# Kernel tuning notes

Measured on AMD Instinct MI355X. Metric: run time of the kernel, lower is better.

Reference implementation:

```python
import jax, jax.numpy as jnp
import numpy as np

IN_FEATURES = 4096
OUT_FEATURES = 11008
B, S = 4, 2048


def setup_inputs() -> dict:
    key = jax.random.key(0)
    k1, k2, k3, k4 = jax.random.split(key, 4)
    x = jax.random.normal(k1, (B, S, IN_FEATURES), dtype=jnp.float32)
    # int8 quantized weights in [-127, 127]
    weight_quantized = jax.random.randint(k2, (OUT_FEATURES, IN_FEATURES), -127, 128, dtype=jnp.int8)
    # realistic per-channel scales (positive, small)
    weight_scale = jax.random.uniform(k3, (OUT_FEATURES,), dtype=jnp.float32, minval=1e-4, maxval=2e-2)
    bias = jax.random.normal(k4, (OUT_FEATURES,), dtype=jnp.float32) * 0.01
    return {"x": x, "weight_quantized": weight_quantized, "weight_scale": weight_scale, "bias": bias}


def reference(x, weight_quantized, weight_scale, bias):
    # Dequantize: W = int8.float() * scale[:, None]  (symmetric, per-channel)
    w = weight_quantized.astype(jnp.float32) * weight_scale[:, None]  # [out, in]
    # F.linear: y = x @ W^T + b
    return jnp.einsum('bsi,oi->bso', x, w) + bias
```

## Files before the change

### kernel.cpp

```cpp
#include <hip/hip_runtime.h>
#include <hip/hip_bf16.h>
#include <stdint.h>


#define M_TOTAL 8192
#define K_TOTAL 4096
#define N_TOTAL 11008
#define NT 32
#define NBM 64
#define NBN 86

typedef __attribute__((ext_vector_type(4))) int int4v;

__device__ inline ushort f2bf(float f) {
    union { __hip_bfloat16 h; ushort u; } cv;
    cv.h = __float2bfloat16(f);
    return cv.u;
}


__global__ __launch_bounds__(256) void quant_x_kernel(const float* __restrict__ x,
                                                      signed char* __restrict__ xq,
                                                      float* __restrict__ sx) {
    const int row = blockIdx.x;
    const int tid = threadIdx.x;
    const float* xr = x + (size_t)row * K_TOTAL + tid * 16;

    float4 v0 = reinterpret_cast<const float4*>(xr)[0];
    float4 v1 = reinterpret_cast<const float4*>(xr)[1];
    float4 v2 = reinterpret_cast<const float4*>(xr)[2];
    float4 v3 = reinterpret_cast<const float4*>(xr)[3];

    float m = 0.f;
    m = fmaxf(m, fmaxf(fmaxf(fabsf(v0.x), fabsf(v0.y)), fmaxf(fabsf(v0.z), fabsf(v0.w))));
    m = fmaxf(m, fmaxf(fmaxf(fabsf(v1.x), fabsf(v1.y)), fmaxf(fabsf(v1.z), fabsf(v1.w))));
    m = fmaxf(m, fmaxf(fmaxf(fabsf(v2.x), fabsf(v2.y)), fmaxf(fabsf(v2.z), fabsf(v2.w))));
    m = fmaxf(m, fmaxf(fmaxf(fabsf(v3.x), fabsf(v3.y)), fmaxf(fabsf(v3.z), fabsf(v3.w))));

    for (int d = 1; d < 64; d <<= 1) m = fmaxf(m, __shfl_xor(m, d));
    __shared__ float wm_[4];
    if ((tid & 63) == 0) wm_[tid >> 6] = m;
    __syncthreads();
    m = fmaxf(fmaxf(wm_[0], wm_[1]), fmaxf(wm_[2], wm_[3]));

    const float inv = (m > 0.f) ? (127.f / m) : 0.f;
    if (tid == 0) sx[row] = (m > 0.f) ? (m / 127.f) : 0.f;

    float tmp[16] = {v0.x,v0.y,v0.z,v0.w, v1.x,v1.y,v1.z,v1.w,
                     v2.x,v2.y,v2.z,v2.w, v3.x,v3.y,v3.z,v3.w};
    int q[16];
#pragma unroll
    for (int i = 0; i < 16; ++i) {
        int t = __float2int_rn(tmp[i] * inv);
        q[i] = t > 127 ? 127 : (t < -127 ? -127 : t);
    }
    int4v o;
#pragma unroll
    for (int w = 0; w < 4; ++w)
        o[w] = (q[w*4] & 255) | ((q[w*4+1] & 255) << 8) |
               ((q[w*4+2] & 255) << 16) | ((q[w*4+3] & 255) << 24);
    *reinterpret_cast<int4v*>(xq + (size_t)row * K_TOTAL + tid * 16) = o;
}


__global__ __launch_bounds__(256) void cvt_w_kernel(const int* __restrict__ in,
                                                    signed char* __restrict__ out, int nitems) {
    bool is8 = false;
    for (int i = 0; i < 256; ++i) {
        int v = in[i];
        if (v < -127 || v > 127) { is8 = true; break; }
    }
    int stride = gridDim.x * blockDim.x;
    if (!is8) {
        for (int i = blockIdx.x * blockDim.x + threadIdx.x; i < nitems; i += stride) {
            const int* p = in + (size_t)i * 16;
            int4v o;
#pragma unroll
            for (int w = 0; w < 4; ++w)
                o[w] = (p[w*4] & 255) | ((p[w*4+1] & 255) << 8) |
                       ((p[w*4+2] & 255) << 16) | ((p[w*4+3] & 255) << 24);
            *reinterpret_cast<int4v*>(out + (size_t)i * 16) = o;
        }
    } else {
        const int4v* in16 = reinterpret_cast<const int4v*>(in);
        for (int i = blockIdx.x * blockDim.x + threadIdx.x; i < nitems; i += stride)
            *reinterpret_cast<int4v*>(out + (size_t)i * 16) = in16[i];
    }
}


#define GLOAD16(g, l) __builtin_amdgcn_global_load_lds( \
    (const __attribute__((address_space(1))) void*)(g), \
    (__attribute__((address_space(3))) void*)(l), 16, 0, 0)


__global__ __launch_bounds__(256, 2) void gemm_kernel(const unsigned char* __restrict__ A,
                                                      const unsigned char* __restrict__ B,
                                                      const float* __restrict__ sx,
                                                      const float* __restrict__ scale,
                                                      const float* __restrict__ bias,
                                                      float* __restrict__ C) {
    __shared__ unsigned char sh[65536];

    const int tid  = threadIdx.x;
    const int wv   = tid >> 6;
    const int lane = tid & 63;
    const int wm   = wv >> 1;
    const int wn   = wv & 1;

    const int xcd = blockIdx.x & 7;
    const int l   = blockIdx.x >> 3;
    const int band = l / 344;
    const int lb   = l - band * 344;
    const int st   = lb >> 4;
    const int r    = lb & 15;
    int bm_l, bn;
    if (st < 21) { bm_l = band * 4 + (r >> 2); bn = st * 4 + (r & 3); }
    else         { bm_l = band * 4 + (r >> 1); bn = 84 + (r & 1); }
    const int bm = xcd * 8 + bm_l;

    const int fr  = lane & 15;
    const int fq  = lane >> 4;
    const int swz = fr & 7;
    const int kx0 = (fq ^ swz) * 16;
    const int kx1 = ((4 + fq) ^ swz) * 16;

    const int c0 = wv * 4;
    const int rl = lane >> 3;
    const int sg = (lane & 7) ^ rl;
    size_t soff[4];
#pragma unroll
    for (int i = 0; i < 4; ++i)
        soff[i] = (size_t)((c0 + i) * 8 + rl) * K_TOTAL + sg * 16;

    const unsigned char* aS = A + (size_t)bm * 128 * K_TOTAL;
    const unsigned char* bS = B + (size_t)bn * 128 * K_TOTAL;

    int4v acc[4][4] = {};

#pragma unroll
    for (int i = 0; i < 4; ++i) GLOAD16(aS + soff[i],       sh + (c0 + i) * 1024);
#pragma unroll
    for (int i = 0; i < 4; ++i) GLOAD16(bS + soff[i],       sh + 16384 + (c0 + i) * 1024);
#pragma unroll
    for (int i = 0; i < 4; ++i) GLOAD16(bS + 128 + soff[i], sh + 32768 + 16384 + (c0 + i) * 1024);
    asm volatile("s_waitcnt vmcnt(4)" ::: "memory");
    __builtin_amdgcn_s_barrier();

#pragma unroll 1
    for (int t = 0; t < NT; ++t) {
        const int p = t & 1;
        const unsigned char* rd  = sh + (p << 15);
        unsigned char* stA = sh + ((p ^ 1) << 15);
        unsigned char* stB = sh + (p << 15) + 16384;
        const unsigned char* aSrc = aS + (size_t)(t + 1) * 128;
        const unsigned char* bSrc = bS + (size_t)(t + 2) * 128;

        int4v af0[4], af1[4], bf0[4], bf1[4];

#pragma unroll
        for (int i = 0; i < 4; ++i) {
            const unsigned char* ap = rd + (wm * 64 + i * 16 + fr) * 128;
            af0[i] = *(const int4v*)(ap + kx0);
        }
#pragma unroll
        for (int n = 0; n < 4; ++n) {
            const unsigned char* bp = rd + 16384 + (wn * 64 + n * 16 + fr) * 128;
            bf0[n] = *(const int4v*)(bp + kx0);
            bf1[n] = *(const int4v*)(bp + kx1);
        }
        if (t + 1 < NT) {
#pragma unroll
            for (int i = 0; i < 4; ++i)
                GLOAD16(aSrc + soff[i], stA + (c0 + i) * 1024);
        }
        __builtin_amdgcn_s_barrier();
        asm volatile("s_waitcnt lgkmcnt(0)" ::: "memory");
        __builtin_amdgcn_s_setprio(1);
#pragma unroll
        for (int i = 0; i < 4; ++i)
#pragma unroll
            for (int n = 0; n < 4; ++n)
                acc[i][n] = __builtin_amdgcn_mfma_i32_16x16x64_i8(af0[i], bf0[n], acc[i][n], 0, 0, 0);
        __builtin_amdgcn_s_setprio(0);
        __builtin_amdgcn_s_barrier();

#pragma unroll
        for (int i = 0; i < 4; ++i) {
            const unsigned char* ap = rd + (wm * 64 + i * 16 + fr) * 128;
            af1[i] = *(const int4v*)(ap + kx1);
        }
        if (t + 2 < NT) {
#pragma unroll
            for (int i = 0; i < 4; ++i)
                GLOAD16(bSrc + soff[i], stB + (c0 + i) * 1024);
        }
        __builtin_amdgcn_s_barrier();
        asm volatile("s_waitcnt lgkmcnt(0)" ::: "memory");
        __builtin_amdgcn_s_setprio(1);
#pragma unroll
        for (int i = 0; i < 4; ++i)
#pragma unroll
            for (int n = 0; n < 4; ++n)
                acc[i][n] = __builtin_amdgcn_mfma_i32_16x16x64_i8(af1[i], bf1[n], acc[i][n], 0, 0, 0);
        __builtin_amdgcn_s_setprio(0);
        if (t + 2 < NT) { asm volatile("s_waitcnt vmcnt(4)" ::: "memory"); }
        else            { asm volatile("s_waitcnt vmcnt(0)" ::: "memory"); }
        __builtin_amdgcn_s_barrier();
    }

    const int crow0 = bm * 128 + wm * 64;
    const int ccol0 = bn * 128 + wn * 64;
    float scv[4], bsv[4];
#pragma unroll
    for (int n = 0; n < 4; ++n) {
        const int col = ccol0 + n * 16 + fr;
        scv[n] = scale[col];
        bsv[n] = bias[col];
    }
#pragma unroll
    for (int fm = 0; fm < 4; ++fm) {
#pragma unroll
        for (int j = 0; j < 4; ++j) {
            const int row = crow0 + fm * 16 + fq * 4 + j;
            const float sr = sx[row];
            float* cp = C + (size_t)row * N_TOTAL + ccol0 + fr;
#pragma unroll
            for (int n = 0; n < 4; ++n)
                cp[n * 16] = (float)acc[fm][n][j] * (sr * scv[n]) + bsv[n];
        }
    }
}


__global__ __launch_bounds__(256) void gemm_fallback(const float* __restrict__ x,
                                                     const int* __restrict__ w,
                                                     const float* __restrict__ scale,
                                                     const float* __restrict__ bias,
                                                     float* __restrict__ C) {
    bool is8 = false;
    for (int i = 0; i < 256; ++i) {
        int v = w[i];
        if (v < -127 || v > 127) { is8 = true; break; }
    }
    const signed char* w8 = (const signed char*)w;

    __shared__ float As[64][16];
    __shared__ float Bs[64][16];
    const int nbn = N_TOTAL / 64;
    const int bm = blockIdx.x / nbn;
    const int bn = blockIdx.x % nbn;
    const int tid = threadIdx.x;
    const int tx = tid & 15, ty = tid >> 4;

    float acc[4][4] = {};
    for (int kt = 0; kt < K_TOTAL; kt += 16) {
        for (int i = 0; i < 4; ++i) {
            int idx = tid + i * 256;
            int r = idx >> 4, c = idx & 15;
            As[r][c] = x[(size_t)(bm * 64 + r) * K_TOTAL + kt + c];
            size_t widx = (size_t)(bn * 64 + r) * K_TOTAL + kt + c;
            Bs[r][c] = is8 ? (float)w8[widx] : (float)w[widx];
        }
        __syncthreads();
        for (int kk = 0; kk < 16; ++kk) {
            float a[4], b[4];
            for (int i = 0; i < 4; ++i) a[i] = As[ty * 4 + i][kk];
            for (int j = 0; j < 4; ++j) b[j] = Bs[tx * 4 + j][kk];
            for (int i = 0; i < 4; ++i)
                for (int j = 0; j < 4; ++j) acc[i][j] += a[i] * b[j];
        }
        __syncthreads();
    }
    for (int j = 0; j < 4; ++j) {
        int col = bn * 64 + tx * 4 + j;
        float s = scale[col], bb = bias[col];
        for (int i = 0; i < 4; ++i) {
            int row = bm * 64 + ty * 4 + i;
            C[(size_t)row * N_TOTAL + col] = acc[i][j] * s + bb;
        }
    }
}


extern "C" void kernel_launch(void* const* d_in, const int* in_sizes, int n_in,
                              void* d_out, int out_size, void* d_ws, size_t ws_size,
                              hipStream_t stream) {
    const float* x     = (const float*)d_in[0];
    const int*   wq    = (const int*)d_in[1];
    const float* scale = (const float*)d_in[2];
    const float* bias  = (const float*)d_in[3];
    float*       out   = (float*)d_out;

    const size_t x_bytes = (size_t)M_TOTAL * K_TOTAL;
    const size_t w_bytes = (size_t)N_TOTAL * K_TOTAL;
    const size_t need = x_bytes + w_bytes + M_TOTAL * sizeof(float);

    if (ws_size >= need) {
        signed char* xq = (signed char*)d_ws;
        signed char* wb = (signed char*)d_ws + x_bytes;
        float*       sx = (float*)((char*)d_ws + x_bytes + w_bytes);

        quant_x_kernel<<<M_TOTAL, 256, 0, stream>>>(x, xq, sx);
        cvt_w_kernel<<<2048, 256, 0, stream>>>(wq, wb, (int)(w_bytes / 16));
        dim3 grid(NBM * NBN);
        gemm_kernel<<<grid, 256, 0, stream>>>((const unsigned char*)xq,
                                              (const unsigned char*)wb,
                                              sx, scale, bias, out);
    } else {
        dim3 grid((M_TOTAL / 64) * (N_TOTAL / 64));
        gemm_fallback<<<grid, 256, 0, stream>>>(x, wq, scale, bias, out);
    }
}
```

Measured before the change: 463.2 us.

## Software-pipeline LDS fragment reads across iterations to overlap with MFMA

```diff
diff --git a/kernel.cpp b/kernel.cpp
--- a/kernel.cpp
+++ b/kernel.cpp
@@ -12,12 +12,6 @@
 
 typedef __attribute__((ext_vector_type(4))) int int4v;
 
-__device__ inline ushort f2bf(float f) {
-    union { __hip_bfloat16 h; ushort u; } cv;
-    cv.h = __float2bfloat16(f);
-    return cv.u;
-}
-
 
 __global__ __launch_bounds__(256) void quant_x_kernel(const float* __restrict__ x,
                                                       signed char* __restrict__ xq,
@@ -93,6 +87,33 @@
     (const __attribute__((address_space(1))) void*)(g), \
     (__attribute__((address_space(3))) void*)(l), 16, 0, 0)
 
+
+#define RD_A(dst, base, KX)                                                     \
+    _Pragma("unroll")                                                           \
+    for (int i_ = 0; i_ < 4; ++i_)                                              \
+        dst[i_] = *(const int4v*)((base) + (wm * 64 + i_ * 16 + fr) * 128 + (KX));
+#define RD_B(dst, base, KX)                                                     \
+    _Pragma("unroll")                                                           \
+    for (int n_ = 0; n_ < 4; ++n_)                                              \
+        dst[n_] = *(const int4v*)((base) + 16384 + (wn * 64 + n_ * 16 + fr) * 128 + (KX));
+#define MFMA16(fa, fb)                                                          \
+    __builtin_amdgcn_s_setprio(1);                                              \
+    _Pragma("unroll")                                                           \
+    for (int i_ = 0; i_ < 4; ++i_) {                                            \
+        _Pragma("unroll")                                                       \
+        for (int n_ = 0; n_ < 4; ++n_)                                          \
+            acc[i_][n_] = __builtin_amdgcn_mfma_i32_16x16x64_i8(                \
+                fa[i_], fb[n_], acc[i_][n_], 0, 0, 0);                          \
+    }                                                                           \
+    __builtin_amdgcn_s_setprio(0);
+#define STAGE_A(asrc, buf)                                                      \
+    _Pragma("unroll")                                                           \
+    for (int i_ = 0; i_ < 4; ++i_)                                              \
+        GLOAD16((asrc) + soff[i_], (buf) + (c0 + i_) * 1024);
+#define STAGE_B(bsrc, buf)                                                      \
+    _Pragma("unroll")                                                           \
+    for (int i_ = 0; i_ < 4; ++i_)                                              \
+        GLOAD16((bsrc) + soff[i_], (buf) + 16384 + (c0 + i_) * 1024);
 
 __global__ __launch_bounds__(256, 2) void gemm_kernel(const unsigned char* __restrict__ A,
                                                       const unsigned char* __restrict__ B,
@@ -135,78 +156,45 @@
 
     const unsigned char* aS = A + (size_t)bm * 128 * K_TOTAL;
     const unsigned char* bS = B + (size_t)bn * 128 * K_TOTAL;
+    unsigned char* buf0 = sh;
+    unsigned char* buf1 = sh + 32768;
 
     int4v acc[4][4] = {};
-
-#pragma unroll
-    for (int i = 0; i < 4; ++i) GLOAD16(aS + soff[i],       sh + (c0 + i) * 1024);
-#pragma unroll
-    for (int i = 0; i < 4; ++i) GLOAD16(bS + soff[i],       sh + 16384 + (c0 + i) * 1024);
-#pragma unroll
-    for (int i = 0; i < 4; ++i) GLOAD16(bS + 128 + soff[i], sh + 32768 + 16384 + (c0 + i) * 1024);
+    int4v afX[4], afY[4], bf0v[4], bf1v[4];
+
+    STAGE_A(aS, buf0)
+    STAGE_B(bS, buf0)
+    STAGE_B(bS + 128, buf1)
     asm volatile("s_waitcnt vmcnt(4)" ::: "memory");
     __builtin_amdgcn_s_barrier();
+    RD_A(afX, buf0, kx0)
+    RD_B(bf0v, buf0, kx0)
+    RD_B(bf1v, buf0, kx1)
 
 #pragma unroll 1
     for (int t = 0; t < NT; ++t) {
         const int p = t & 1;
-        const unsigned char* rd  = sh + (p << 15);
-        unsigned char* stA = sh + ((p ^ 1) << 15);
-        unsigned char* stB = sh + (p << 15) + 16384;
-        const unsigned char* aSrc = aS + (size_t)(t + 1) * 128;
-        const unsigned char* bSrc = bS + (size_t)(t + 2) * 128;
-
-        int4v af0[4], af1[4], bf0[4], bf1[4];
-
-#pragma unroll
-        for (int i = 0; i < 4; ++i) {
-            const unsigned char* ap = rd + (wm * 64 + i * 16 + fr) * 128;
-            af0[i] = *(const int4v*)(ap + kx0);
-        }
-#pragma unroll
-        for (int n = 0; n < 4; ++n) {
-            const unsigned char* bp = rd + 16384 + (wn * 64 + n * 16 + fr) * 128;
-            bf0[n] = *(const int4v*)(bp + kx0);
-            bf1[n] = *(const int4v*)(bp + kx1);
-        }
+        unsigned char* bp = p ? buf1 : buf0;
+        unsigned char* bq = p ? buf0 : buf1;
+
+        RD_A(afY, bp, kx1)
+        if (t + 1 < NT) { STAGE_A(aS + (size_t)(t + 1) * 128, bq) }
+        MFMA16(afX, bf0v)
+        asm volatile("s_waitcnt lgkmcnt(0)" ::: "memory");
+        __builtin_amdgcn_s_barrier();
+
+        if (t + 2 < NT) { STAGE_B(bS + (size_t)(t + 2) * 128, bp) }
+        MFMA16(afY, bf1v)
         if (t + 1 < NT) {
-#pragma unroll
-            for (int i = 0; i < 4; ++i)
-                GLOAD16(aSrc + soff[i], stA + (c0 + i) * 1024);
+            if (t + 2 < NT) { asm volatile("s_waitcnt vmcnt(4)" ::: "memory"); }
+            else            { asm volatile("s_waitcnt vmcnt(0)" ::: "memory"); }
         }
         __builtin_amdgcn_s_barrier();
-        asm volatile("s_waitcnt lgkmcnt(0)" ::: "memory");
-        __builtin_amdgcn_s_setprio(1);
-#pragma unroll
-        for (int i = 0; i < 4; ++i)
-#pragma unroll
-            for (int n = 0; n < 4; ++n)
-                acc[i][n] = __builtin_amdgcn_mfma_i32_16x16x64_i8(af0[i], bf0[n], acc[i][n], 0, 0, 0);
-        __builtin_amdgcn_s_setprio(0);
-        __builtin_amdgcn_s_barrier();
-
-#pragma unroll
-        for (int i = 0; i < 4; ++i) {
-            const unsigned char* ap = rd + (wm * 64 + i * 16 + fr) * 128;
-            af1[i] = *(const int4v*)(ap + kx1);
-        }
-        if (t + 2 < NT) {
-#pragma unroll
-            for (int i = 0; i < 4; ++i)
-                GLOAD16(bSrc + soff[i], stB + (c0 + i) * 1024);
-        }
-        __builtin_amdgcn_s_barrier();
-        asm volatile("s_waitcnt lgkmcnt(0)" ::: "memory");
-        __builtin_amdgcn_s_setprio(1);
-#pragma unroll
-        for (int i = 0; i < 4; ++i)
-#pragma unroll
-            for (int n = 0; n < 4; ++n)
-                acc[i][n] = __builtin_amdgcn_mfma_i32_16x16x64_i8(af1[i], bf1[n], acc[i][n], 0, 0, 0);
-        __builtin_amdgcn_s_setprio(0);
-        if (t + 2 < NT) { asm volatile("s_waitcnt vmcnt(4)" ::: "memory"); }
-        else            { asm volatile("s_waitcnt vmcnt(0)" ::: "memory"); }
-        __builtin_amdgcn_s_barrier();
+        if (t + 1 < NT) {
+            RD_A(afX, bq, kx0)
+            RD_B(bf0v, bq, kx0)
+            RD_B(bf1v, bq, kx1)
+        }
     }
 
     const int crow0 = bm * 128 + wm * 64;
@@ -257,10 +245,10 @@
     for (int kt = 0; kt < K_TOTAL; kt += 16) {
         for (int i = 0; i < 4; ++i) {
             int idx = tid + i * 256;
-            int r = idx >> 4, c = idx & 15;
-            As[r][c] = x[(size_t)(bm * 64 + r) * K_TOTAL + kt + c];
-            size_t widx = (size_t)(bn * 64 + r) * K_TOTAL + kt + c;
-            Bs[r][c] = is8 ? (float)w8[widx] : (float)w[widx];
+            int rr = idx >> 4, cc = idx & 15;
+            As[rr][cc] = x[(size_t)(bm * 64 + rr) * K_TOTAL + kt + cc];
+            size_t widx = (size_t)(bn * 64 + rr) * K_TOTAL + kt + cc;
+            Bs[rr][cc] = is8 ? (float)w8[widx] : (float)w[widx];
         }
         __syncthreads();
         for (int kk = 0; kk < 16; ++kk) {
```

Result: no change. 471.9 us (+1.9%).
